# Optimization experiments

Measured on AMD Instinct MI355X. Metric: run time of the kernel, lower is better.

## Reference

```python
import jax, jax.numpy as jnp
import numpy as np

B, S = 4096, 256
D = 32  # output_size // 4


def setup_inputs() -> dict:
    key = jax.random.key(0)
    ks = jax.random.split(key, 32)
    # continuous features
    cont_p = jax.random.normal(ks[0], (B, S, 3), dtype=jnp.float32)
    cont_c = jax.random.normal(ks[1], (B, S, 2), dtype=jnp.float32)
    # categorical features, per-column vocab sizes from Embedding tables
    vocabs_p = [2, 2, 2, 11, 34]
    cat_p = jnp.stack([
        jax.random.randint(ks[2 + i], (B, S), 0, v, dtype=jnp.int32)
        for i, v in enumerate(vocabs_p)], axis=2)
    vocabs_c = [19, 31]
    cat_c = jnp.stack([
        jax.random.randint(ks[7 + i], (B, S), 0, v, dtype=jnp.int32)
        for i, v in enumerate(vocabs_c)], axis=2)
    lengths = jax.random.randint(ks[9], (B,), 1, S + 1, dtype=jnp.int32)

    def lin(k, fan_in, fan_out):
        bound = 1.0 / np.sqrt(fan_in)
        kw, kb = jax.random.split(k)
        w = jax.random.uniform(kw, (fan_in, fan_out), jnp.float32, -bound, bound)
        b = jax.random.uniform(kb, (fan_out,), jnp.float32, -bound, bound)
        return w, b

    w_p1, b_p1 = lin(ks[10], 3, D)
    w_p2, b_p2 = lin(ks[11], D, D)
    w_c1, b_c1 = lin(ks[12], 2, D)
    w_c2, b_c2 = lin(ks[13], D, D)
    emb_gender = jax.random.normal(ks[14], (2, D), dtype=jnp.float32)
    emb_korean = jax.random.normal(ks[15], (2, D), dtype=jnp.float32)
    emb_primary = jax.random.normal(ks[16], (2, D), dtype=jnp.float32)
    emb_job = jax.random.normal(ks[17], (11, D), dtype=jnp.float32)
    emb_rep = jax.random.normal(ks[18], (34, D), dtype=jnp.float32)
    emb_place = jax.random.normal(ks[19], (19, D), dtype=jnp.float32)
    emb_add = jax.random.normal(ks[20], (31, D), dtype=jnp.float32)
    w_fc1, b_fc1 = lin(ks[21], 128, 64)
    w_fc2, b_fc2 = lin(ks[22], 64, 2)

    return dict(cont_p=cont_p, cont_c=cont_c, cat_p=cat_p, cat_c=cat_c,
                lengths=lengths,
                w_p1=w_p1, b_p1=b_p1, w_p2=w_p2, b_p2=b_p2,
                w_c1=w_c1, b_c1=b_c1, w_c2=w_c2, b_c2=b_c2,
                emb_gender=emb_gender, emb_korean=emb_korean,
                emb_primary=emb_primary, emb_job=emb_job, emb_rep=emb_rep,
                emb_place=emb_place, emb_add=emb_add,
                w_fc1=w_fc1, b_fc1=b_fc1, w_fc2=w_fc2, b_fc2=b_fc2)


def reference(cont_p, cont_c, cat_p, cat_c, lengths,
              w_p1, b_p1, w_p2, b_p2, w_c1, b_c1, w_c2, b_c2,
              emb_gender, emb_korean, emb_primary, emb_job, emb_rep,
              emb_place, emb_add, w_fc1, b_fc1, w_fc2, b_fc2):
    # small per-token MLPs on continuous features -> [B,S,D]
    hp = jax.nn.relu(cont_p @ w_p1 + b_p1) @ w_p2 + b_p2
    hc = jax.nn.relu(cont_c @ w_c1 + b_c1) @ w_c2 + b_c2
    # multi-table embedding lookups, averaged per group -> [B,S,D]
    ep = (emb_gender[cat_p[:, :, 0]] + emb_korean[cat_p[:, :, 1]] +
          emb_primary[cat_p[:, :, 2]] + emb_job[cat_p[:, :, 3]] +
          emb_rep[cat_p[:, :, 4]]) / 5.0
    ec = (emb_place[cat_c[:, :, 0]] + emb_add[cat_c[:, :, 1]]) / 2.0
    # concat order matches torch: (cat_p, cat_c, cont_p, cont_c) -> [B,S,128]
    x = jnp.concatenate([ep, ec, hp, hc], axis=2)
    # ragged mean pool over first lengths[i] positions (masked segment mean)
    mask = (jnp.arange(x.shape[1])[None, :] < lengths[:, None])
    pooled = jnp.sum(x * mask[:, :, None], axis=1) / lengths[:, None].astype(x.dtype)
    # head: relu(fc1) -> relu(fc2); dropout p=0.0 is identity
    h = jax.nn.relu(pooled @ w_fc1 + b_fc1)
    return jax.nn.relu(h @ w_fc2 + b_fc2)
```

## Files before the change

### kernel.cpp

```cpp
#include <hip/hip_runtime.h>


#define BDIM 64

__global__ __launch_bounds__(BDIM)
void mlpreg_kernel(const float* __restrict__ cont_p,
                   const float* __restrict__ cont_c,
                   const int* __restrict__ cat_p,
                   const int* __restrict__ cat_c,
                   const int* __restrict__ lengths,
                   const float* __restrict__ w_p1, const float* __restrict__ b_p1,
                   const float* __restrict__ w_p2, const float* __restrict__ b_p2,
                   const float* __restrict__ w_c1, const float* __restrict__ b_c1,
                   const float* __restrict__ w_c2, const float* __restrict__ b_c2,
                   const float* __restrict__ emb_g,  const float* __restrict__ emb_k,
                   const float* __restrict__ emb_pr, const float* __restrict__ emb_j,
                   const float* __restrict__ emb_r,  const float* __restrict__ emb_pl,
                   const float* __restrict__ emb_a,
                   const float* __restrict__ w_fc1, const float* __restrict__ b_fc1,
                   const float* __restrict__ w_fc2, const float* __restrict__ b_fc2,
                   float* __restrict__ out)
{
    constexpr int S = 256;
    __shared__ float sP[2][S * 3];
    __shared__ float sC[2][S * 2];
    __shared__ int   hist[2][96];
    __shared__ float sPacc[2][64];
    __shared__ float sPool[2][128];

    const int lane = threadIdx.x;
    const int b0 = blockIdx.x * 2, b1 = b0 + 1;

    int L0 = lengths[b0]; L0 = (L0 < 1) ? 1 : (L0 > S ? S : L0);
    int L1 = lengths[b1]; L1 = (L1 < 1) ? 1 : (L1 > S ? S : L1);
    const float L0f = (float)L0, L1f = (float)L1;
    const float invL0 = 1.0f / L0f, invL1 = 1.0f / L1f;

    { int i = lane;            ((int*)hist)[i] = 0;
      i += 64;                 ((int*)hist)[i] = 0;
      i += 64;                 ((int*)hist)[i] = 0; }

    const int ch = lane & 31, h = lane >> 5;
    const float wp0 = w_p1[ch], wp1 = w_p1[32 + ch], wp2 = w_p1[64 + ch], bp = b_p1[ch];
    const float wc0 = w_c1[ch], wc1 = w_c1[32 + ch], bc = b_c1[ch];

    {
        const float4* gp0 = (const float4*)(cont_p + (size_t)b0 * (S * 3));
        const float4* gp1 = (const float4*)(cont_p + (size_t)b1 * (S * 3));
        const float4* gc0 = (const float4*)(cont_c + (size_t)b0 * (S * 2));
        const float4* gc1 = (const float4*)(cont_c + (size_t)b1 * (S * 2));
        const int n0 = (3 * L0 + 3) >> 2, n1 = (3 * L1 + 3) >> 2;
        const int m0 = (2 * L0 + 3) >> 2, m1 = (2 * L1 + 3) >> 2;
        for (int i = lane; i < n0; i += 64) *(float4*)&sP[0][4 * i] = gp0[i];
        for (int i = lane; i < n1; i += 64) *(float4*)&sP[1][4 * i] = gp1[i];
        for (int i = lane; i < m0; i += 64) *(float4*)&sC[0][4 * i] = gc0[i];
        for (int i = lane; i < m1; i += 64) *(float4*)&sC[1][4 * i] = gc1[i];
    }

    int sg0 = 0, sk0 = 0, sp0 = 0, sg1 = 0, sk1 = 0, sp1 = 0;
    {
        const int*  kp0 = cat_p + (size_t)b0 * (S * 5);
        const int*  kp1 = cat_p + (size_t)b1 * (S * 5);
        const int2* kc0 = (const int2*)(cat_c + (size_t)b0 * (S * 2));
        const int2* kc1 = (const int2*)(cat_c + (size_t)b1 * (S * 2));
        #pragma unroll 2
        for (int t = lane; t < L0; t += 64) {
            int v0 = kp0[5 * t], v1 = kp0[5 * t + 1], v2 = kp0[5 * t + 2],
                v3 = kp0[5 * t + 3], v4 = kp0[5 * t + 4];
            int2 q = kc0[t];
            sg0 += v0; sk0 += v1; sp0 += v2;
            atomicAdd(&hist[0][v3], 1);
            atomicAdd(&hist[0][11 + v4], 1);
            atomicAdd(&hist[0][45 + q.x], 1);
            atomicAdd(&hist[0][64 + q.y], 1);
        }
        #pragma unroll 2
        for (int t = lane; t < L1; t += 64) {
            int v0 = kp1[5 * t], v1 = kp1[5 * t + 1], v2 = kp1[5 * t + 2],
                v3 = kp1[5 * t + 3], v4 = kp1[5 * t + 4];
            int2 q = kc1[t];
            sg1 += v0; sk1 += v1; sp1 += v2;
            atomicAdd(&hist[1][v3], 1);
            atomicAdd(&hist[1][11 + v4], 1);
            atomicAdd(&hist[1][45 + q.x], 1);
            atomicAdd(&hist[1][64 + q.y], 1);
        }
    }
    #pragma unroll
    for (int d = 32; d; d >>= 1) {
        sg0 += __shfl_xor(sg0, d); sk0 += __shfl_xor(sk0, d); sp0 += __shfl_xor(sp0, d);
        sg1 += __shfl_xor(sg1, d); sk1 += __shfl_xor(sk1, d); sp1 += __shfl_xor(sp1, d);
    }
    __syncthreads();

    {
        const int   Lr   = h ? L1 : L0;
        const float invr = h ? invL1 : invL0;
        const float* tp = sP[h];
        const float* tc = sC[h];
        float aP = 0.f, aC = 0.f;
        #pragma unroll 4
        for (int t = 0; t < Lr; ++t) {
            float c0 = tp[3 * t], c1 = tp[3 * t + 1], c2 = tp[3 * t + 2];
            float2 d2 = *(const float2*)&tc[2 * t];
            aP += fmaxf(fmaf(c0, wp0, fmaf(c1, wp1, fmaf(c2, wp2, bp))), 0.f);
            aC += fmaxf(fmaf(d2.x, wc0, fmaf(d2.y, wc1, bc)), 0.f);
        }
        sPacc[h][ch]      = aP * invr;
        sPacc[h][32 + ch] = aC * invr;
    }
    __syncthreads();

    if (h == 0) {
        float g0 = emb_g[ch],  g1 = emb_g[32 + ch];
        float k0 = emb_k[ch],  k1 = emb_k[32 + ch];
        float p0 = emb_pr[ch], p1 = emb_pr[32 + ch];
        float fg0 = (float)sg0, fk0 = (float)sk0, fp0 = (float)sp0;
        float fg1 = (float)sg1, fk1 = (float)sk1, fp1 = (float)sp1;
        float A0 = fmaf(L0f - fg0, g0, fg0 * g1) + fmaf(L0f - fk0, k0, fk0 * k1)
                 + fmaf(L0f - fp0, p0, fp0 * p1);
        float A1 = fmaf(L1f - fg1, g0, fg1 * g1) + fmaf(L1f - fk1, k0, fk1 * k1)
                 + fmaf(L1f - fp1, p0, fp1 * p1);
        #pragma unroll
        for (int r = 0; r < 11; ++r) {
            float w = emb_j[r * 32 + ch];
            A0 = fmaf((float)hist[0][r], w, A0);
            A1 = fmaf((float)hist[1][r], w, A1);
        }
        #pragma unroll
        for (int r = 0; r < 34; ++r) {
            float w = emb_r[r * 32 + ch];
            A0 = fmaf((float)hist[0][11 + r], w, A0);
            A1 = fmaf((float)hist[1][11 + r], w, A1);
        }
        sPool[0][ch] = A0 * (invL0 * 0.2f);
        sPool[1][ch] = A1 * (invL1 * 0.2f);

        float v0 = b_p2[ch], v1 = v0;
        #pragma unroll
        for (int k = 0; k < 32; ++k) {
            float w = w_p2[k * 32 + ch];
            v0 = fmaf(sPacc[0][k], w, v0);
            v1 = fmaf(sPacc[1][k], w, v1);
        }
        sPool[0][64 + ch] = v0;
        sPool[1][64 + ch] = v1;
    } else {
        float A0 = 0.f, A1 = 0.f;
        #pragma unroll
        for (int r = 0; r < 19; ++r) {
            float w = emb_pl[r * 32 + ch];
            A0 = fmaf((float)hist[0][45 + r], w, A0);
            A1 = fmaf((float)hist[1][45 + r], w, A1);
        }
        #pragma unroll
        for (int r = 0; r < 31; ++r) {
            float w = emb_a[r * 32 + ch];
            A0 = fmaf((float)hist[0][64 + r], w, A0);
            A1 = fmaf((float)hist[1][64 + r], w, A1);
        }
        sPool[0][32 + ch] = A0 * (invL0 * 0.5f);
        sPool[1][32 + ch] = A1 * (invL1 * 0.5f);

        float v0 = b_c2[ch], v1 = v0;
        #pragma unroll
        for (int k = 0; k < 32; ++k) {
            float w = w_c2[k * 32 + ch];
            v0 = fmaf(sPacc[0][32 + k], w, v0);
            v1 = fmaf(sPacc[1][32 + k], w, v1);
        }
        sPool[0][96 + ch] = v0;
        sPool[1][96 + ch] = v1;
    }
    __syncthreads();

    {
        const int o = lane;
        float x0 = b_fc1[o], y0 = 0.f;
        float x1 = x0,       y1 = 0.f;
        #pragma unroll 8
        for (int k = 0; k < 128; k += 2) {
            float wa = w_fc1[(size_t)k * 64 + o];
            float wb = w_fc1[(size_t)(k + 1) * 64 + o];
            float u0 = sPool[0][k], u1 = sPool[0][k + 1];
            float s0 = sPool[1][k], s1 = sPool[1][k + 1];
            x0 = fmaf(u0, wa, x0); y0 = fmaf(u1, wb, y0);
            x1 = fmaf(s0, wa, x1); y1 = fmaf(s1, wb, y1);
        }
        float h0 = fmaxf(x0 + y0, 0.f);
        float h1 = fmaxf(x1 + y1, 0.f);
        float wa = w_fc2[2 * o], wb = w_fc2[2 * o + 1];
        float q00 = h0 * wa, q01 = h0 * wb, q10 = h1 * wa, q11 = h1 * wb;
        #pragma unroll
        for (int d = 32; d; d >>= 1) {
            q00 += __shfl_xor(q00, d); q01 += __shfl_xor(q01, d);
            q10 += __shfl_xor(q10, d); q11 += __shfl_xor(q11, d);
        }
        if (lane == 0) {
            float bb0 = b_fc2[0], bb1 = b_fc2[1];
            float4 o4;
            o4.x = fmaxf(q00 + bb0, 0.f);
            o4.y = fmaxf(q01 + bb1, 0.f);
            o4.z = fmaxf(q10 + bb0, 0.f);
            o4.w = fmaxf(q11 + bb1, 0.f);
            *(float4*)&out[(size_t)b0 * 2] = o4;
        }
    }
}

extern "C" void kernel_launch(void* const* d_in, const int* in_sizes, int n_in,
                              void* d_out, int out_size, void* d_ws, size_t ws_size,
                              hipStream_t stream) {
    const float* cont_p = (const float*)d_in[0];
    const float* cont_c = (const float*)d_in[1];
    const int*   cat_p  = (const int*)d_in[2];
    const int*   cat_c  = (const int*)d_in[3];
    const int*   lens   = (const int*)d_in[4];
    const float* w_p1   = (const float*)d_in[5];
    const float* b_p1   = (const float*)d_in[6];
    const float* w_p2   = (const float*)d_in[7];
    const float* b_p2   = (const float*)d_in[8];
    const float* w_c1   = (const float*)d_in[9];
    const float* b_c1   = (const float*)d_in[10];
    const float* w_c2   = (const float*)d_in[11];
    const float* b_c2   = (const float*)d_in[12];
    const float* emb_g  = (const float*)d_in[13];
    const float* emb_k  = (const float*)d_in[14];
    const float* emb_pr = (const float*)d_in[15];
    const float* emb_j  = (const float*)d_in[16];
    const float* emb_r  = (const float*)d_in[17];
    const float* emb_pl = (const float*)d_in[18];
    const float* emb_a  = (const float*)d_in[19];
    const float* w_fc1  = (const float*)d_in[20];
    const float* b_fc1  = (const float*)d_in[21];
    const float* w_fc2  = (const float*)d_in[22];
    const float* b_fc2  = (const float*)d_in[23];
    float* out = (float*)d_out;

    hipLaunchKernelGGL(mlpreg_kernel, dim3(2048), dim3(BDIM), 0, stream,
                       cont_p, cont_c, cat_p, cat_c, lens,
                       w_p1, b_p1, w_p2, b_p2, w_c1, b_c1, w_c2, b_c2,
                       emb_g, emb_k, emb_pr, emb_j, emb_r, emb_pl, emb_a,
                       w_fc1, b_fc1, w_fc2, b_fc2, out);
}
```

Baseline: 142.7 us.

## Process one batch row per block and read continuous features directly from global

```diff
diff --git a/kernel.cpp b/kernel.cpp
--- a/kernel.cpp
+++ b/kernel.cpp
@@ -3,7 +3,7 @@
 
 #define BDIM 64
 
-__global__ __launch_bounds__(BDIM)
+__global__ __launch_bounds__(BDIM, 4)
 void mlpreg_kernel(const float* __restrict__ cont_p,
                    const float* __restrict__ cont_c,
                    const int* __restrict__ cat_p,
@@ -22,188 +22,119 @@
                    float* __restrict__ out)
 {
     constexpr int S = 256;
-    __shared__ float sP[2][S * 3];
-    __shared__ float sC[2][S * 2];
-    __shared__ int   hist[2][96];
-    __shared__ float sPacc[2][64];
-    __shared__ float sPool[2][128];
+    __shared__ int   hist[96];
+    __shared__ float sAcc[64];
+    __shared__ float sPool[128];
 
     const int lane = threadIdx.x;
-    const int b0 = blockIdx.x * 2, b1 = b0 + 1;
+    const int b = blockIdx.x;
+    const int ch = lane & 31, h = lane >> 5;
 
-    int L0 = lengths[b0]; L0 = (L0 < 1) ? 1 : (L0 > S ? S : L0);
-    int L1 = lengths[b1]; L1 = (L1 < 1) ? 1 : (L1 > S ? S : L1);
-    const float L0f = (float)L0, L1f = (float)L1;
-    const float invL0 = 1.0f / L0f, invL1 = 1.0f / L1f;
+    int L = lengths[b]; L = (L < 1) ? 1 : (L > S ? S : L);
+    const float Lf = (float)L, invL = 1.0f / Lf;
 
-    { int i = lane;            ((int*)hist)[i] = 0;
-      i += 64;                 ((int*)hist)[i] = 0;
-      i += 64;                 ((int*)hist)[i] = 0; }
+    hist[lane] = 0;
+    if (lane < 32) hist[64 + lane] = 0;
 
-    const int ch = lane & 31, h = lane >> 5;
     const float wp0 = w_p1[ch], wp1 = w_p1[32 + ch], wp2 = w_p1[64 + ch], bp = b_p1[ch];
     const float wc0 = w_c1[ch], wc1 = w_c1[32 + ch], bc = b_c1[ch];
 
+    int sg = 0, sk = 0, sp = 0;
     {
-        const float4* gp0 = (const float4*)(cont_p + (size_t)b0 * (S * 3));
-        const float4* gp1 = (const float4*)(cont_p + (size_t)b1 * (S * 3));
-        const float4* gc0 = (const float4*)(cont_c + (size_t)b0 * (S * 2));
-        const float4* gc1 = (const float4*)(cont_c + (size_t)b1 * (S * 2));
-        const int n0 = (3 * L0 + 3) >> 2, n1 = (3 * L1 + 3) >> 2;
-        const int m0 = (2 * L0 + 3) >> 2, m1 = (2 * L1 + 3) >> 2;
-        for (int i = lane; i < n0; i += 64) *(float4*)&sP[0][4 * i] = gp0[i];
-        for (int i = lane; i < n1; i += 64) *(float4*)&sP[1][4 * i] = gp1[i];
-        for (int i = lane; i < m0; i += 64) *(float4*)&sC[0][4 * i] = gc0[i];
-        for (int i = lane; i < m1; i += 64) *(float4*)&sC[1][4 * i] = gc1[i];
+        const int*  kp = cat_p + (size_t)b * (S * 5);
+        const int2* kc = (const int2*)(cat_c + (size_t)b * (S * 2));
+        #pragma unroll 2
+        for (int t = lane; t < L; t += 64) {
+            int v0 = kp[5 * t], v1 = kp[5 * t + 1], v2 = kp[5 * t + 2],
+                v3 = kp[5 * t + 3], v4 = kp[5 * t + 4];
+            int2 q = kc[t];
+            sg += v0; sk += v1; sp += v2;
+            atomicAdd(&hist[v3], 1);
+            atomicAdd(&hist[11 + v4], 1);
+            atomicAdd(&hist[45 + q.x], 1);
+            atomicAdd(&hist[64 + q.y], 1);
+        }
     }
 
-    int sg0 = 0, sk0 = 0, sp0 = 0, sg1 = 0, sk1 = 0, sp1 = 0;
+    float aP = 0.f, aC = 0.f;
     {
-        const int*  kp0 = cat_p + (size_t)b0 * (S * 5);
-        const int*  kp1 = cat_p + (size_t)b1 * (S * 5);
-        const int2* kc0 = (const int2*)(cat_c + (size_t)b0 * (S * 2));
-        const int2* kc1 = (const int2*)(cat_c + (size_t)b1 * (S * 2));
-        #pragma unroll 2
-        for (int t = lane; t < L0; t += 64) {
-            int v0 = kp0[5 * t], v1 = kp0[5 * t + 1], v2 = kp0[5 * t + 2],
-                v3 = kp0[5 * t + 3], v4 = kp0[5 * t + 4];
-            int2 q = kc0[t];
-            sg0 += v0; sk0 += v1; sp0 += v2;
-            atomicAdd(&hist[0][v3], 1);
-            atomicAdd(&hist[0][11 + v4], 1);
-            atomicAdd(&hist[0][45 + q.x], 1);
-            atomicAdd(&hist[0][64 + q.y], 1);
-        }
-        #pragma unroll 2
-        for (int t = lane; t < L1; t += 64) {
-            int v0 = kp1[5 * t], v1 = kp1[5 * t + 1], v2 = kp1[5 * t + 2],
-                v3 = kp1[5 * t + 3], v4 = kp1[5 * t + 4];
-            int2 q = kc1[t];
-            sg1 += v0; sk1 += v1; sp1 += v2;
-            atomicAdd(&hist[1][v3], 1);
-            atomicAdd(&hist[1][11 + v4], 1);
-            atomicAdd(&hist[1][45 + q.x], 1);
-            atomicAdd(&hist[1][64 + q.y], 1);
-        }
-    }
-    #pragma unroll
-    for (int d = 32; d; d >>= 1) {
-        sg0 += __shfl_xor(sg0, d); sk0 += __shfl_xor(sk0, d); sp0 += __shfl_xor(sp0, d);
-        sg1 += __shfl_xor(sg1, d); sk1 += __shfl_xor(sk1, d); sp1 += __shfl_xor(sp1, d);
-    }
-    __syncthreads();
-
-    {
-        const int   Lr   = h ? L1 : L0;
-        const float invr = h ? invL1 : invL0;
-        const float* tp = sP[h];
-        const float* tc = sC[h];
-        float aP = 0.f, aC = 0.f;
+        const float* tp = cont_p + (size_t)b * (S * 3);
+        const float* tc = cont_c + (size_t)b * (S * 2);
         #pragma unroll 4
-        for (int t = 0; t < Lr; ++t) {
+        for (int t = h; t < L; t += 2) {
             float c0 = tp[3 * t], c1 = tp[3 * t + 1], c2 = tp[3 * t + 2];
             float2 d2 = *(const float2*)&tc[2 * t];
             aP += fmaxf(fmaf(c0, wp0, fmaf(c1, wp1, fmaf(c2, wp2, bp))), 0.f);
             aC += fmaxf(fmaf(d2.x, wc0, fmaf(d2.y, wc1, bc)), 0.f);
         }
-        sPacc[h][ch]      = aP * invr;
-        sPacc[h][32 + ch] = aC * invr;
     }
+    aP += __shfl_xor(aP, 32);
+    aC += __shfl_xor(aC, 32);
+    #pragma unroll
+    for (int d = 32; d; d >>= 1) {
+        sg += __shfl_xor(sg, d); sk += __shfl_xor(sk, d); sp += __shfl_xor(sp, d);
+    }
+
+    sAcc[lane] = (h ? aC : aP) * invL;
     __syncthreads();
 
-    if (h == 0) {
+    float A;
+    {
+        float fg = (float)sg, fk = (float)sk, fp = (float)sp;
         float g0 = emb_g[ch],  g1 = emb_g[32 + ch];
         float k0 = emb_k[ch],  k1 = emb_k[32 + ch];
         float p0 = emb_pr[ch], p1 = emb_pr[32 + ch];
-        float fg0 = (float)sg0, fk0 = (float)sk0, fp0 = (float)sp0;
-        float fg1 = (float)sg1, fk1 = (float)sk1, fp1 = (float)sp1;
-        float A0 = fmaf(L0f - fg0, g0, fg0 * g1) + fmaf(L0f - fk0, k0, fk0 * k1)
-                 + fmaf(L0f - fp0, p0, fp0 * p1);
-        float A1 = fmaf(L1f - fg1, g0, fg1 * g1) + fmaf(L1f - fk1, k0, fk1 * k1)
-                 + fmaf(L1f - fp1, p0, fp1 * p1);
-        #pragma unroll
-        for (int r = 0; r < 11; ++r) {
-            float w = emb_j[r * 32 + ch];
-            A0 = fmaf((float)hist[0][r], w, A0);
-            A1 = fmaf((float)hist[1][r], w, A1);
+        A = fmaf(Lf - fg, g0, fg * g1) + fmaf(Lf - fk, k0, fk * k1)
+          + fmaf(Lf - fp, p0, fp * p1);
+        A = h ? 0.f : A;
+    }
+    {
+        const float* tA = h ? emb_pl : emb_j;
+        const float* tB = h ? emb_a  : emb_r;
+        const int nA = h ? 19 : 11;
+        const int nT = h ? 50 : 45;
+        const int hb = h ? 45 : 0;
+        #pragma unroll 5
+        for (int r = 0; r < nT; ++r) {
+            const float* p = (r < nA) ? (tA + (r << 5)) : (tB + ((r - nA) << 5));
+            A = fmaf((float)hist[hb + r], p[ch], A);
         }
-        #pragma unroll
-        for (int r = 0; r < 34; ++r) {
-            float w = emb_r[r * 32 + ch];
-            A0 = fmaf((float)hist[0][11 + r], w, A0);
-            A1 = fmaf((float)hist[1][11 + r], w, A1);
-        }
-        sPool[0][ch] = A0 * (invL0 * 0.2f);
-        sPool[1][ch] = A1 * (invL1 * 0.2f);
-
-        float v0 = b_p2[ch], v1 = v0;
-        #pragma unroll
-        for (int k = 0; k < 32; ++k) {
-            float w = w_p2[k * 32 + ch];
-            v0 = fmaf(sPacc[0][k], w, v0);
-            v1 = fmaf(sPacc[1][k], w, v1);
-        }
-        sPool[0][64 + ch] = v0;
-        sPool[1][64 + ch] = v1;
-    } else {
-        float A0 = 0.f, A1 = 0.f;
-        #pragma unroll
-        for (int r = 0; r < 19; ++r) {
-            float w = emb_pl[r * 32 + ch];
-            A0 = fmaf((float)hist[0][45 + r], w, A0);
-            A1 = fmaf((float)hist[1][45 + r], w, A1);
-        }
-        #pragma unroll
-        for (int r = 0; r < 31; ++r) {
-            float w = emb_a[r * 32 + ch];
-            A0 = fmaf((float)hist[0][64 + r], w, A0);
-            A1 = fmaf((float)hist[1][64 + r], w, A1);
-        }
-        sPool[0][32 + ch] = A0 * (invL0 * 0.5f);
-        sPool[1][32 + ch] = A1 * (invL1 * 0.5f);
-
-        float v0 = b_c2[ch], v1 = v0;
-        #pragma unroll
-        for (int k = 0; k < 32; ++k) {
-            float w = w_c2[k * 32 + ch];
-            v0 = fmaf(sPacc[0][32 + k], w, v0);
-            v1 = fmaf(sPacc[1][32 + k], w, v1);
-        }
-        sPool[0][96 + ch] = v0;
-        sPool[1][96 + ch] = v1;
+        sPool[(h << 5) + ch] = A * (invL * (h ? 0.5f : 0.2f));
+    }
+    {
+        const float* W2 = h ? w_c2 : w_p2;
+        float v = (h ? b_c2 : b_p2)[ch];
+        const float* acc = &sAcc[h << 5];
+        #pragma unroll 8
+        for (int k = 0; k < 32; ++k)
+            v = fmaf(acc[k], W2[(k << 5) + ch], v);
+        sPool[64 + (h << 5) + ch] = v;
     }
     __syncthreads();
 
     {
-        const int o = lane;
-        float x0 = b_fc1[o], y0 = 0.f;
-        float x1 = x0,       y1 = 0.f;
+        float x = b_fc1[lane], y = 0.f;
         #pragma unroll 8
-        for (int k = 0; k < 128; k += 2) {
-            float wa = w_fc1[(size_t)k * 64 + o];
-            float wb = w_fc1[(size_t)(k + 1) * 64 + o];
-            float u0 = sPool[0][k], u1 = sPool[0][k + 1];
-            float s0 = sPool[1][k], s1 = sPool[1][k + 1];
-            x0 = fmaf(u0, wa, x0); y0 = fmaf(u1, wb, y0);
-            x1 = fmaf(s0, wa, x1); y1 = fmaf(s1, wb, y1);
+        for (int k = 0; k < 128; k += 4) {
+            float4 u = *(const float4*)&sPool[k];
+            float w0 = w_fc1[(size_t)(k    ) * 64 + lane];
+            float w1 = w_fc1[(size_t)(k + 1) * 64 + lane];
+            float w2 = w_fc1[(size_t)(k + 2) * 64 + lane];
+            float w3 = w_fc1[(size_t)(k + 3) * 64 + lane];
+            x = fmaf(u.x, w0, x); y = fmaf(u.y, w1, y);
+            x = fmaf(u.z, w2, x); y = fmaf(u.w, w3, y);
         }
-        float h0 = fmaxf(x0 + y0, 0.f);
-        float h1 = fmaxf(x1 + y1, 0.f);
-        float wa = w_fc2[2 * o], wb = w_fc2[2 * o + 1];
-        float q00 = h0 * wa, q01 = h0 * wb, q10 = h1 * wa, q11 = h1 * wb;
+        float hv = fmaxf(x + y, 0.f);
+        float q0 = hv * w_fc2[2 * lane], q1 = hv * w_fc2[2 * lane + 1];
         #pragma unroll
         for (int d = 32; d; d >>= 1) {
-            q00 += __shfl_xor(q00, d); q01 += __shfl_xor(q01, d);
-            q10 += __shfl_xor(q10, d); q11 += __shfl_xor(q11, d);
+            q0 += __shfl_xor(q0, d); q1 += __shfl_xor(q1, d);
         }
         if (lane == 0) {
-            float bb0 = b_fc2[0], bb1 = b_fc2[1];
-            float4 o4;
-            o4.x = fmaxf(q00 + bb0, 0.f);
-            o4.y = fmaxf(q01 + bb1, 0.f);
-            o4.z = fmaxf(q10 + bb0, 0.f);
-            o4.w = fmaxf(q11 + bb1, 0.f);
-            *(float4*)&out[(size_t)b0 * 2] = o4;
+            float2 o2;
+            o2.x = fmaxf(q0 + b_fc2[0], 0.f);
+            o2.y = fmaxf(q1 + b_fc2[1], 0.f);
+            *(float2*)&out[(size_t)b * 2] = o2;
         }
     }
 }
@@ -237,7 +168,7 @@
     const float* b_fc2  = (const float*)d_in[23];
     float* out = (float*)d_out;
 
-    hipLaunchKernelGGL(mlpreg_kernel, dim3(2048), dim3(BDIM), 0, stream,
+    hipLaunchKernelGGL(mlpreg_kernel, dim3(4096), dim3(BDIM), 0, stream,
                        cont_p, cont_c, cat_p, cat_c, lens,
                        w_p1, b_p1, w_p2, b_p2, w_c1, b_c1, w_c2, b_c2,
                        emb_g, emb_k, emb_pr, emb_j, emb_r, emb_pl, emb_a,
```

New measurement: 155.2 us. 8.8% more time.
